# Optimization experiments

Hardware: AMD Instinct MI355X
Metric: run time of the kernel (lower is better)

## Reference

```python
import jax, jax.numpy as jnp
import numpy as np

EPS = 1e-7  # K.epsilon()

def squash(v, axis=-1):
    # scale = |v|^2 / (1+|v|^2) / |v|
    ss = jnp.sum(jnp.square(v), axis=axis, keepdims=True)
    scale = ss / (1.0 + ss) / jnp.sqrt(ss + EPS)
    return scale * v

def setup_inputs() -> dict:
    key = jax.random.key(0)
    k1, k2 = jax.random.split(key)
    B, IN_CAPS, IN_DIM = 64, 512, 128
    N_CAPS, OUT_DIM = 16, 32
    inputs = jax.random.normal(k1, (B, IN_CAPS, IN_DIM), dtype=jnp.float32)
    # glorot-uniform-like init for W: (in_caps, n_caps, in_dim, out_dim)
    limit = np.sqrt(6.0 / (IN_DIM + OUT_DIM))
    W = jax.random.uniform(k2, (IN_CAPS, N_CAPS, IN_DIM, OUT_DIM),
                           minval=-limit, maxval=limit, dtype=jnp.float32)
    return {"inputs": inputs, "W": W, "num_routing": 3}

def reference(inputs, W, num_routing):
    # Prediction vectors u_hat[b,i,j,d] = sum_k inputs[b,i,k] * W[i,j,k,d]
    u_hat = jnp.einsum('bik,ijkd->bijd', inputs, W)
    B, IN_CAPS, N_CAPS, _ = u_hat.shape
    b = jnp.zeros((B, IN_CAPS, N_CAPS), dtype=u_hat.dtype)
    outputs = None
    for r in range(num_routing):  # small fixed iteration count
        c = jax.nn.softmax(b, axis=2)                     # coupling coeffs over output caps
        s = jnp.einsum('bij,bijd->bjd', c, u_hat)         # weighted sum over input caps
        outputs = squash(s)                               # (B, n_caps, out_dim)
        if r < num_routing - 1:
            b = b + jnp.einsum('bjd,bijd->bij', outputs, u_hat)  # agreement update
    return outputs
```

## Files before the change

### kernel.cpp

```cpp
#include <hip/hip_runtime.h>

typedef unsigned short u16;
typedef unsigned int u32;
typedef unsigned long long u64;
typedef __attribute__((ext_vector_type(8))) short short8;
typedef __attribute__((ext_vector_type(4))) float f32x4;

#define ICAPS 512
#define IDIM 128
#define NFLAT 512

__device__ __forceinline__ float b2f(u16 h) {
    union { u32 u; float f; } x; x.u = ((u32)h) << 16; return x.f;
}
__device__ __forceinline__ u16 f2b(float f) {
    union { float f; u32 u; } x; x.f = f;
    return (u16)((x.u + 0x7FFFu + ((x.u >> 16) & 1u)) >> 16);
}

__global__ __launch_bounds__(256, 4) void gemm_kernel(const float* __restrict__ x,
                                                      const float* __restrict__ W,
                                                      u16* __restrict__ uhat) {
    __shared__ __align__(16) u16 As[64 * 136];
    const int i = blockIdx.x >> 2;
    const int chunk = blockIdx.x & 3;
    const int t = threadIdx.x;

    {
        const float4* xa = (const float4*)x;
        float4 av[8];
        #pragma unroll
        for (int l = 0; l < 8; ++l) {
            int id = l * 256 + t;
            av[l] = xa[(size_t)((id >> 5) * ICAPS + i) * 32 + (id & 31)];
        }
        #pragma unroll
        for (int l = 0; l < 8; ++l) {
            int id = l * 256 + t;
            int row = id >> 5, kq = id & 31;
            union { u16 h[4]; u64 q; } pk;
            pk.h[0] = f2b(av[l].x); pk.h[1] = f2b(av[l].y);
            pk.h[2] = f2b(av[l].z); pk.h[3] = f2b(av[l].w);
            *(u64*)&As[row * 136 + kq * 4] = pk.q;
        }
    }
    __syncthreads();

    const int lane = t & 63;
    const int w = t >> 6;
    const int ln = lane & 15;
    const int q = lane >> 4;

    const float* colbase[2];
    #pragma unroll
    for (int nt = 0; nt < 2; ++nt) {
        int c = (2 * w + nt) * 16 + ln;
        int jj = c >> 5, d = c & 31;
        colbase[nt] = W + (size_t)(i * 16 + chunk * 4 + jj) * 128 * 32 + d;
    }

    f32x4 acc[4][2] = {};
    #pragma unroll
    for (int ks = 0; ks < 4; ++ks) {
        const int ko = ks * 32 + q * 8;
        short8 a[4], bb[2];
        #pragma unroll
        for (int mt = 0; mt < 4; ++mt)
            a[mt] = *(const short8*)&As[(mt * 16 + ln) * 136 + ko];
        #pragma unroll
        for (int nt = 0; nt < 2; ++nt) {
            const float* p = colbase[nt] + (size_t)ko * 32;
            float wv[8];
            #pragma unroll
            for (int e = 0; e < 8; ++e) wv[e] = p[e * 32];
            #pragma unroll
            for (int e = 0; e < 8; ++e) bb[nt][e] = (short)f2b(wv[e]);
        }
        #pragma unroll
        for (int mt = 0; mt < 4; ++mt)
            #pragma unroll
            for (int nt = 0; nt < 2; ++nt)
                acc[mt][nt] = __builtin_amdgcn_mfma_f32_16x16x32_bf16(a[mt], bb[nt], acc[mt][nt], 0, 0, 0);
    }
    #pragma unroll
    for (int mt = 0; mt < 4; ++mt)
        #pragma unroll
        for (int nt = 0; nt < 2; ++nt) {
            int n = chunk * 128 + (2 * w + nt) * 16 + ln;
            #pragma unroll
            for (int r = 0; r < 4; ++r) {
                int brow = mt * 16 + q * 4 + r;
                uhat[((size_t)brow * ICAPS + i) * NFLAT + n] = f2b(acc[mt][nt][r]);
            }
        }
}

__global__ __launch_bounds__(256) void p0_kernel(const u16* __restrict__ uhat,
                                                 float* __restrict__ q0) {
    __shared__ __align__(16) float red[4][NFLAT];
    const int b = blockIdx.x >> 4;
    const int ch = blockIdx.x & 15;
    const int t = threadIdx.x;
    const int wv = t >> 6, l = t & 63;
    float acc[8] = {0.f, 0.f, 0.f, 0.f, 0.f, 0.f, 0.f, 0.f};
    for (int ii = 0; ii < 8; ++ii) {
        int i = ch * 32 + wv * 8 + ii;
        union { uint4 v; u16 h[8]; } tmp;
        tmp.v = *(const uint4*)&uhat[((size_t)b * ICAPS + i) * NFLAT + l * 8];
        #pragma unroll
        for (int e = 0; e < 8; ++e) acc[e] += b2f(tmp.h[e]);
    }
    #pragma unroll
    for (int e = 0; e < 8; ++e) red[wv][l * 8 + e] = acc[e];
    __syncthreads();
    q0[(size_t)blockIdx.x * NFLAT + t] =
        red[0][t] + red[1][t] + red[2][t] + red[3][t];
    q0[(size_t)blockIdx.x * NFLAT + 256 + t] =
        red[0][t + 256] + red[1][t + 256] + red[2][t + 256] + red[3][t + 256];
}

__global__ __launch_bounds__(256) void combine_kernel(const float* __restrict__ q,
                                                      float* __restrict__ s) {
    const int b = blockIdx.x, t = threadIdx.x;
    #pragma unroll
    for (int rep = 0; rep < 2; ++rep) {
        int n = rep * 256 + t;
        float acc = 0.f;
        #pragma unroll
        for (int ch = 0; ch < 16; ++ch)
            acc += q[(size_t)(b * 16 + ch) * NFLAT + n];
        s[b * NFLAT + n] = acc;
    }
}

__device__ __forceinline__ void squash_osum(const float* __restrict__ s0,
                                            const float* __restrict__ s1,
                                            float* __restrict__ osum,
                                            int b, int t, int use1) {
    const int j = t >> 4, g = t & 15;
    const int n0 = j * 32 + 2 * g;
    float v0 = s0[b * NFLAT + n0] * 0.0625f;
    float v1 = s0[b * NFLAT + n0 + 1] * 0.0625f;
    float p = v0 * v0 + v1 * v1;
    p += __shfl_xor(p, 1); p += __shfl_xor(p, 2);
    p += __shfl_xor(p, 4); p += __shfl_xor(p, 8);
    float sc = (p / (1.f + p)) / sqrtf(p + 1e-7f);
    float o0 = sc * v0, o1 = sc * v1;
    if (use1) {
        float w0 = s1[b * NFLAT + n0];
        float w1 = s1[b * NFLAT + n0 + 1];
        float pq = w0 * w0 + w1 * w1;
        pq += __shfl_xor(pq, 1); pq += __shfl_xor(pq, 2);
        pq += __shfl_xor(pq, 4); pq += __shfl_xor(pq, 8);
        float sc1 = (pq / (1.f + pq)) / sqrtf(pq + 1e-7f);
        o0 += sc1 * w0; o1 += sc1 * w1;
    }
    osum[n0] = o0; osum[n0 + 1] = o1;
}

__global__ __launch_bounds__(256) void route_kernel(const u16* __restrict__ uhat,
                                                    const float* __restrict__ s0,
                                                    const float* __restrict__ s1,
                                                    float* __restrict__ qout,
                                                    int use1) {
    __shared__ float osum[NFLAT];
    __shared__ __align__(16) float red[4][NFLAT];
    const int b = blockIdx.x >> 4;
    const int ch = blockIdx.x & 15;
    const int t = threadIdx.x;
    squash_osum(s0, s1, osum, b, t, use1);
    __syncthreads();
    const int wv = t >> 6, l = t & 63;
    float os[8], acc[8];
    #pragma unroll
    for (int e = 0; e < 8; ++e) { os[e] = osum[l * 8 + e]; acc[e] = 0.f; }
    for (int ii = 0; ii < 8; ++ii) {
        int i = ch * 32 + wv * 8 + ii;
        union { uint4 v; u16 h[8]; } tmp;
        tmp.v = *(const uint4*)&uhat[((size_t)b * ICAPS + i) * NFLAT + l * 8];
        float u[8];
        #pragma unroll
        for (int e = 0; e < 8; ++e) u[e] = b2f(tmp.h[e]);
        float d = 0.f;
        #pragma unroll
        for (int e = 0; e < 8; ++e) d += u[e] * os[e];
        d += __shfl_xor(d, 1); d += __shfl_xor(d, 2);
        float mx = d;
        mx = fmaxf(mx, __shfl_xor(mx, 4));  mx = fmaxf(mx, __shfl_xor(mx, 8));
        mx = fmaxf(mx, __shfl_xor(mx, 16)); mx = fmaxf(mx, __shfl_xor(mx, 32));
        float ex = __expf(d - mx);
        float ss = ex;
        ss += __shfl_xor(ss, 4);  ss += __shfl_xor(ss, 8);
        ss += __shfl_xor(ss, 16); ss += __shfl_xor(ss, 32);
        float c = ex / ss;
        #pragma unroll
        for (int e = 0; e < 8; ++e) acc[e] += c * u[e];
    }
    #pragma unroll
    for (int e = 0; e < 8; ++e) red[wv][l * 8 + e] = acc[e];
    __syncthreads();
    qout[(size_t)blockIdx.x * NFLAT + t] =
        red[0][t] + red[1][t] + red[2][t] + red[3][t];
    qout[(size_t)blockIdx.x * NFLAT + 256 + t] =
        red[0][t + 256] + red[1][t + 256] + red[2][t + 256] + red[3][t + 256];
}

__global__ __launch_bounds__(256) void fin_kernel(const float* __restrict__ q2,
                                                  float* __restrict__ out) {
    const int b = blockIdx.x, t = threadIdx.x;
    const int j = t >> 4, g = t & 15;
    const int n0 = j * 32 + 2 * g;
    float v0 = 0.f, v1 = 0.f;
    #pragma unroll
    for (int ch = 0; ch < 16; ++ch) {
        v0 += q2[(size_t)(b * 16 + ch) * NFLAT + n0];
        v1 += q2[(size_t)(b * 16 + ch) * NFLAT + n0 + 1];
    }
    float p = v0 * v0 + v1 * v1;
    p += __shfl_xor(p, 1); p += __shfl_xor(p, 2);
    p += __shfl_xor(p, 4); p += __shfl_xor(p, 8);
    float sc = (p / (1.f + p)) / sqrtf(p + 1e-7f);
    out[b * NFLAT + n0]     = sc * v0;
    out[b * NFLAT + n0 + 1] = sc * v1;
}

extern "C" void kernel_launch(void* const* d_in, const int* in_sizes, int n_in,
                              void* d_out, int out_size, void* d_ws, size_t ws_size,
                              hipStream_t stream) {
    const float* x = nullptr;
    const float* W = nullptr;
    for (int a = 0; a < n_in; ++a) {
        if (in_sizes[a] == 64 * 512 * 128) x = (const float*)d_in[a];
        else if (in_sizes[a] == 512 * 16 * 128 * 32) W = (const float*)d_in[a];
    }
    if (!x) x = (const float*)d_in[0];
    if (!W) W = (const float*)d_in[1];

    char* ws = (char*)d_ws;
    const size_t U = 2ull * 64 * 512 * 512;
    u16*   uhat = (u16*)ws;
    float* q0 = (float*)(ws + U);
    float* q1 = (float*)(ws + U + (2ull << 20));
    float* q2 = (float*)(ws + U + (4ull << 20));
    float* s0 = (float*)(ws + U + (6ull << 20));
    float* s1 = (float*)(ws + U + (6ull << 20) + (128ull << 10));
    float* out = (float*)d_out;

    hipLaunchKernelGGL(gemm_kernel, dim3(2048), dim3(256), 0, stream, x, W, uhat);
    hipLaunchKernelGGL(p0_kernel, dim3(1024), dim3(256), 0, stream, uhat, q0);
    hipLaunchKernelGGL(combine_kernel, dim3(64), dim3(256), 0, stream, q0, s0);
    hipLaunchKernelGGL(route_kernel, dim3(1024), dim3(256), 0, stream, uhat, s0, s0, q1, 0);
    hipLaunchKernelGGL(combine_kernel, dim3(64), dim3(256), 0, stream, q1, s1);
    hipLaunchKernelGGL(route_kernel, dim3(1024), dim3(256), 0, stream, uhat, s0, s1, q2, 1);
    hipLaunchKernelGGL(fin_kernel, dim3(64), dim3(256), 0, stream, q2, out);
}
```

Measured before the change: 245.9 us.

## Coalesce GEMM epilogue via LDS and fuse all routing iterations into one kernel

The GEMM epilogue now stages the bf16 results in shared memory, then writes them out as 16-byte vectors. This replaces the scattered 2-byte global stores of u_hat. The six routing, combine and finalize launches are replaced by a single kernel with one 1024-thread block per batch element, which does the reductions, squash and softmax routing entirely in shared memory. This removes the partial-sum buffers and the launch overhead, but it runs only 64 blocks, which may underuse the device while streaming u_hat three times.

```diff
diff --git a/kernel.cpp b/kernel.cpp
--- a/kernel.cpp
+++ b/kernel.cpp
@@ -82,146 +82,126 @@
             for (int nt = 0; nt < 2; ++nt)
                 acc[mt][nt] = __builtin_amdgcn_mfma_f32_16x16x32_bf16(a[mt], bb[nt], acc[mt][nt], 0, 0, 0);
     }
+
+    __syncthreads();
     #pragma unroll
     for (int mt = 0; mt < 4; ++mt)
         #pragma unroll
         for (int nt = 0; nt < 2; ++nt) {
-            int n = chunk * 128 + (2 * w + nt) * 16 + ln;
+            int nl = (2 * w + nt) * 16 + ln;
             #pragma unroll
             for (int r = 0; r < 4; ++r) {
                 int brow = mt * 16 + q * 4 + r;
-                uhat[((size_t)brow * ICAPS + i) * NFLAT + n] = f2b(acc[mt][nt][r]);
+                As[brow * 136 + nl] = f2b(acc[mt][nt][r]);
             }
         }
-}
-
-__global__ __launch_bounds__(256) void p0_kernel(const u16* __restrict__ uhat,
-                                                 float* __restrict__ q0) {
-    __shared__ __align__(16) float red[4][NFLAT];
-    const int b = blockIdx.x >> 4;
-    const int ch = blockIdx.x & 15;
+    __syncthreads();
+    #pragma unroll
+    for (int p = 0; p < 4; ++p) {
+        int brow = p * 16 + (t >> 4);
+        int col8 = (t & 15) * 8;
+        uint4 v = *(const uint4*)&As[brow * 136 + col8];
+        *(uint4*)&uhat[((size_t)brow * ICAPS + i) * NFLAT + chunk * 128 + col8] = v;
+    }
+}
+
+__global__ __launch_bounds__(1024, 1) void route_all(const u16* __restrict__ uhat,
+                                                     float* __restrict__ out) {
+    __shared__ __align__(16) float red[16][NFLAT];
+    __shared__ float sbuf[NFLAT];
+    __shared__ float osum[NFLAT];
+    const int b = blockIdx.x;
     const int t = threadIdx.x;
     const int wv = t >> 6, l = t & 63;
-    float acc[8] = {0.f, 0.f, 0.f, 0.f, 0.f, 0.f, 0.f, 0.f};
-    for (int ii = 0; ii < 8; ++ii) {
-        int i = ch * 32 + wv * 8 + ii;
+    const u16* ubase = uhat + ((size_t)b * ICAPS + (size_t)wv * 32) * NFLAT + l * 8;
+
+    float acc[8];
+
+    #pragma unroll
+    for (int e = 0; e < 8; ++e) acc[e] = 0.f;
+    #pragma unroll 4
+    for (int ii = 0; ii < 32; ++ii) {
         union { uint4 v; u16 h[8]; } tmp;
-        tmp.v = *(const uint4*)&uhat[((size_t)b * ICAPS + i) * NFLAT + l * 8];
+        tmp.v = *(const uint4*)&ubase[(size_t)ii * NFLAT];
         #pragma unroll
         for (int e = 0; e < 8; ++e) acc[e] += b2f(tmp.h[e]);
     }
     #pragma unroll
     for (int e = 0; e < 8; ++e) red[wv][l * 8 + e] = acc[e];
     __syncthreads();
-    q0[(size_t)blockIdx.x * NFLAT + t] =
-        red[0][t] + red[1][t] + red[2][t] + red[3][t];
-    q0[(size_t)blockIdx.x * NFLAT + 256 + t] =
-        red[0][t + 256] + red[1][t + 256] + red[2][t + 256] + red[3][t + 256];
-}
-
-__global__ __launch_bounds__(256) void combine_kernel(const float* __restrict__ q,
-                                                      float* __restrict__ s) {
-    const int b = blockIdx.x, t = threadIdx.x;
-    #pragma unroll
-    for (int rep = 0; rep < 2; ++rep) {
-        int n = rep * 256 + t;
-        float acc = 0.f;
-        #pragma unroll
-        for (int ch = 0; ch < 16; ++ch)
-            acc += q[(size_t)(b * 16 + ch) * NFLAT + n];
-        s[b * NFLAT + n] = acc;
-    }
-}
-
-__device__ __forceinline__ void squash_osum(const float* __restrict__ s0,
-                                            const float* __restrict__ s1,
-                                            float* __restrict__ osum,
-                                            int b, int t, int use1) {
-    const int j = t >> 4, g = t & 15;
-    const int n0 = j * 32 + 2 * g;
-    float v0 = s0[b * NFLAT + n0] * 0.0625f;
-    float v1 = s0[b * NFLAT + n0 + 1] * 0.0625f;
-    float p = v0 * v0 + v1 * v1;
-    p += __shfl_xor(p, 1); p += __shfl_xor(p, 2);
-    p += __shfl_xor(p, 4); p += __shfl_xor(p, 8);
-    float sc = (p / (1.f + p)) / sqrtf(p + 1e-7f);
-    float o0 = sc * v0, o1 = sc * v1;
-    if (use1) {
-        float w0 = s1[b * NFLAT + n0];
-        float w1 = s1[b * NFLAT + n0 + 1];
-        float pq = w0 * w0 + w1 * w1;
-        pq += __shfl_xor(pq, 1); pq += __shfl_xor(pq, 2);
-        pq += __shfl_xor(pq, 4); pq += __shfl_xor(pq, 8);
-        float sc1 = (pq / (1.f + pq)) / sqrtf(pq + 1e-7f);
-        o0 += sc1 * w0; o1 += sc1 * w1;
-    }
-    osum[n0] = o0; osum[n0 + 1] = o1;
-}
-
-__global__ __launch_bounds__(256) void route_kernel(const u16* __restrict__ uhat,
-                                                    const float* __restrict__ s0,
-                                                    const float* __restrict__ s1,
-                                                    float* __restrict__ qout,
-                                                    int use1) {
-    __shared__ float osum[NFLAT];
-    __shared__ __align__(16) float red[4][NFLAT];
-    const int b = blockIdx.x >> 4;
-    const int ch = blockIdx.x & 15;
-    const int t = threadIdx.x;
-    squash_osum(s0, s1, osum, b, t, use1);
-    __syncthreads();
-    const int wv = t >> 6, l = t & 63;
-    float os[8], acc[8];
-    #pragma unroll
-    for (int e = 0; e < 8; ++e) { os[e] = osum[l * 8 + e]; acc[e] = 0.f; }
-    for (int ii = 0; ii < 8; ++ii) {
-        int i = ch * 32 + wv * 8 + ii;
-        union { uint4 v; u16 h[8]; } tmp;
-        tmp.v = *(const uint4*)&uhat[((size_t)b * ICAPS + i) * NFLAT + l * 8];
-        float u[8];
-        #pragma unroll
-        for (int e = 0; e < 8; ++e) u[e] = b2f(tmp.h[e]);
-        float d = 0.f;
-        #pragma unroll
-        for (int e = 0; e < 8; ++e) d += u[e] * os[e];
-        d += __shfl_xor(d, 1); d += __shfl_xor(d, 2);
-        float mx = d;
-        mx = fmaxf(mx, __shfl_xor(mx, 4));  mx = fmaxf(mx, __shfl_xor(mx, 8));
-        mx = fmaxf(mx, __shfl_xor(mx, 16)); mx = fmaxf(mx, __shfl_xor(mx, 32));
-        float ex = __expf(d - mx);
-        float ss = ex;
-        ss += __shfl_xor(ss, 4);  ss += __shfl_xor(ss, 8);
-        ss += __shfl_xor(ss, 16); ss += __shfl_xor(ss, 32);
-        float c = ex / ss;
-        #pragma unroll
-        for (int e = 0; e < 8; ++e) acc[e] += c * u[e];
-    }
-    #pragma unroll
-    for (int e = 0; e < 8; ++e) red[wv][l * 8 + e] = acc[e];
-    __syncthreads();
-    qout[(size_t)blockIdx.x * NFLAT + t] =
-        red[0][t] + red[1][t] + red[2][t] + red[3][t];
-    qout[(size_t)blockIdx.x * NFLAT + 256 + t] =
-        red[0][t + 256] + red[1][t + 256] + red[2][t + 256] + red[3][t + 256];
-}
-
-__global__ __launch_bounds__(256) void fin_kernel(const float* __restrict__ q2,
-                                                  float* __restrict__ out) {
-    const int b = blockIdx.x, t = threadIdx.x;
-    const int j = t >> 4, g = t & 15;
-    const int n0 = j * 32 + 2 * g;
-    float v0 = 0.f, v1 = 0.f;
-    #pragma unroll
-    for (int ch = 0; ch < 16; ++ch) {
-        v0 += q2[(size_t)(b * 16 + ch) * NFLAT + n0];
-        v1 += q2[(size_t)(b * 16 + ch) * NFLAT + n0 + 1];
-    }
-    float p = v0 * v0 + v1 * v1;
-    p += __shfl_xor(p, 1); p += __shfl_xor(p, 2);
-    p += __shfl_xor(p, 4); p += __shfl_xor(p, 8);
-    float sc = (p / (1.f + p)) / sqrtf(p + 1e-7f);
-    out[b * NFLAT + n0]     = sc * v0;
-    out[b * NFLAT + n0 + 1] = sc * v1;
+    if (t < NFLAT) {
+        float a = 0.f;
+        #pragma unroll
+        for (int w2 = 0; w2 < 16; ++w2) a += red[w2][t];
+        sbuf[t] = a;
+    }
+    __syncthreads();
+    if (t < 256) {
+        const int j = t >> 4, g = t & 15;
+        const int n0 = j * 32 + 2 * g;
+        float v0 = sbuf[n0] * 0.0625f, v1 = sbuf[n0 + 1] * 0.0625f;
+        float p = v0 * v0 + v1 * v1;
+        p += __shfl_xor(p, 1); p += __shfl_xor(p, 2);
+        p += __shfl_xor(p, 4); p += __shfl_xor(p, 8);
+        float sc = (p / (1.f + p)) / sqrtf(p + 1e-7f);
+        osum[n0] = sc * v0; osum[n0 + 1] = sc * v1;
+    }
+    __syncthreads();
+
+    for (int r = 1; r <= 2; ++r) {
+        float os[8];
+        #pragma unroll
+        for (int e = 0; e < 8; ++e) { os[e] = osum[l * 8 + e]; acc[e] = 0.f; }
+        #pragma unroll 2
+        for (int ii = 0; ii < 32; ++ii) {
+            union { uint4 v; u16 h[8]; } tmp;
+            tmp.v = *(const uint4*)&ubase[(size_t)ii * NFLAT];
+            float u[8];
+            #pragma unroll
+            for (int e = 0; e < 8; ++e) u[e] = b2f(tmp.h[e]);
+            float d = 0.f;
+            #pragma unroll
+            for (int e = 0; e < 8; ++e) d += u[e] * os[e];
+            d += __shfl_xor(d, 1); d += __shfl_xor(d, 2);
+            float mx = d;
+            mx = fmaxf(mx, __shfl_xor(mx, 4));  mx = fmaxf(mx, __shfl_xor(mx, 8));
+            mx = fmaxf(mx, __shfl_xor(mx, 16)); mx = fmaxf(mx, __shfl_xor(mx, 32));
+            float ex = __expf(d - mx);
+            float ss = ex;
+            ss += __shfl_xor(ss, 4);  ss += __shfl_xor(ss, 8);
+            ss += __shfl_xor(ss, 16); ss += __shfl_xor(ss, 32);
+            float c = ex / ss;
+            #pragma unroll
+            for (int e = 0; e < 8; ++e) acc[e] += c * u[e];
+        }
+        #pragma unroll
+        for (int e = 0; e < 8; ++e) red[wv][l * 8 + e] = acc[e];
+        __syncthreads();
+        if (t < NFLAT) {
+            float a = 0.f;
+            #pragma unroll
+            for (int w2 = 0; w2 < 16; ++w2) a += red[w2][t];
+            sbuf[t] = a;
+        }
+        __syncthreads();
+        if (t < 256) {
+            const int j = t >> 4, g = t & 15;
+            const int n0 = j * 32 + 2 * g;
+            float w0 = sbuf[n0], w1 = sbuf[n0 + 1];
+            float p = w0 * w0 + w1 * w1;
+            p += __shfl_xor(p, 1); p += __shfl_xor(p, 2);
+            p += __shfl_xor(p, 4); p += __shfl_xor(p, 8);
+            float sc = (p / (1.f + p)) / sqrtf(p + 1e-7f);
+            if (r == 1) {
+                osum[n0]     += sc * w0;
+                osum[n0 + 1] += sc * w1;
+            } else {
+                out[b * NFLAT + n0]     = sc * w0;
+                out[b * NFLAT + n0 + 1] = sc * w1;
+            }
+        }
+        __syncthreads();
+    }
 }
 
 extern "C" void kernel_launch(void* const* d_in, const int* in_sizes, int n_in,
@@ -236,21 +216,9 @@
     if (!x) x = (const float*)d_in[0];
     if (!W) W = (const float*)d_in[1];
 
-    char* ws = (char*)d_ws;
-    const size_t U = 2ull * 64 * 512 * 512;
-    u16*   uhat = (u16*)ws;
-    float* q0 = (float*)(ws + U);
-    float* q1 = (float*)(ws + U + (2ull << 20));
-    float* q2 = (float*)(ws + U + (4ull << 20));
-    float* s0 = (float*)(ws + U + (6ull << 20));
-    float* s1 = (float*)(ws + U + (6ull << 20) + (128ull << 10));
+    u16* uhat = (u16*)d_ws;
     float* out = (float*)d_out;
 
     hipLaunchKernelGGL(gemm_kernel, dim3(2048), dim3(256), 0, stream, x, W, uhat);
-    hipLaunchKernelGGL(p0_kernel, dim3(1024), dim3(256), 0, stream, uhat, q0);
-    hipLaunchKernelGGL(combine_kernel, dim3(64), dim3(256), 0, stream, q0, s0);
-    hipLaunchKernelGGL(route_kernel, dim3(1024), dim3(256), 0, stream, uhat, s0, s0, q1, 0);
-    hipLaunchKernelGGL(combine_kernel, dim3(64), dim3(256), 0, stream, q1, s1);
-    hipLaunchKernelGGL(route_kernel, dim3(1024), dim3(256), 0, stream, uhat, s0, s1, q2, 1);
-    hipLaunchKernelGGL(fin_kernel, dim3(64), dim3(256), 0, stream, q2, out);
-}
+    hipLaunchKernelGGL(route_all, dim3(64), dim3(1024), 0, stream, uhat, out);
+}
```

Result: slower. 253.6 us (+3.1%).
